# Kernel optimization log

Hardware: AMD Instinct MI355X
Metric: run time of the kernel (lower is better)

## Reference

```python
import jax, jax.numpy as jnp
import numpy as np
from jax import lax

B, C, T = 16, 32, 512
GAF_SIZE = 128
LATENT = 128
EPS = 1e-8


def _conv(x, w, b, stride):
    # x: (N, Cin, H, W), w: (Cout, Cin, kh, kw)
    y = lax.conv_general_dilated(x, w, (stride, stride), 'SAME',
                                 dimension_numbers=('NCHW', 'OIHW', 'NCHW'))
    return jax.nn.relu(y + b[None, :, None, None])


def _compute_gaf(x_raw):
    # x_raw: (B, C, T) -> (B*C, 2, S, S) with channels [GASF, GADF]
    S = GAF_SIZE
    # Piecewise Aggregate Approximation: T -> S
    x = x_raw.reshape(B, C, S, T // S).mean(axis=-1)        # (B, C, S)
    # Min-max normalize each series to [-1, 1]
    mn = x.min(axis=-1, keepdims=True)
    mx = x.max(axis=-1, keepdims=True)
    x = jnp.clip(2.0 * (x - mn) / (mx - mn + EPS) - 1.0, -1.0, 1.0)
    # phi = arccos(x); use trig identities to avoid explicit arccos
    sq = jnp.sqrt(jnp.clip(1.0 - x * x, 0.0, 1.0))          # sin(phi)
    xi, xj = x[..., :, None], x[..., None, :]
    si, sj = sq[..., :, None], sq[..., None, :]
    gasf = xi * xj - si * sj                                 # cos(phi_i + phi_j)
    gadf = si * xj - xi * sj                                 # sin(phi_i - phi_j)
    gaf = jnp.stack([gasf, gadf], axis=2)                    # (B, C, 2, S, S)
    return gaf.reshape(B * C, 2, S, S).astype(jnp.float32)


def _encoder(gaf, W1, b1, W2, b2, W3, b3, W4, b4, Wfc, bfc):
    h = _conv(gaf, W1, b1, 2)   # (B*C, 32, 64, 64)
    h = _conv(h, W2, b2, 2)     # (B*C, 64, 32, 32)
    h = _conv(h, W3, b3, 2)     # (B*C, 128, 16, 16)
    h = _conv(h, W4, b4, 2)     # (B*C, 256, 8, 8)
    h = h.mean(axis=(2, 3))     # global average pool -> (B*C, 256)
    return h @ Wfc + bfc        # (B*C, LATENT)


def setup_inputs() -> dict:
    key = jax.random.key(0)
    ks = jax.random.split(key, 12)
    p = lambda k, shp: (jax.random.normal(k, shp, dtype=jnp.float32) * 0.05)
    return {
        'x_raw': jax.random.normal(ks[0], (B, C, T), dtype=jnp.float32),
        'W1': p(ks[1], (32, 2, 3, 3)),   'b1': jnp.zeros((32,), jnp.float32),
        'W2': p(ks[2], (64, 32, 3, 3)),  'b2': jnp.zeros((64,), jnp.float32),
        'W3': p(ks[3], (128, 64, 3, 3)), 'b3': jnp.zeros((128,), jnp.float32),
        'W4': p(ks[4], (256, 128, 3, 3)),'b4': jnp.zeros((256,), jnp.float32),
        'Wfc': p(ks[5], (256, LATENT)),  'bfc': jnp.zeros((LATENT,), jnp.float32),
    }


def reference(x_raw, W1, b1, W2, b2, W3, b3, W4, b4, Wfc, bfc):
    # GAF computed from detached raw EEG in the original (numpy CPU path)
    gaf = lax.stop_gradient(_compute_gaf(x_raw))
    z = _encoder(gaf, W1, b1, W2, b2, W3, b3, W4, b4, Wfc, bfc)
    return z.reshape(B, C, LATENT).mean(axis=1)              # (B, LATENT)
```

## Files before the change

### kernel.cpp

```cpp
#include <hip/hip_runtime.h>
#include <hip/hip_bf16.h>

#define DEV __device__ __forceinline__

constexpr int kB = 16, kC = 32, kT = 512, kS = 128, kBC = 512, kLatent = 128;
constexpr float kEps = 1e-8f;

using bf16 = __hip_bfloat16;
using bf16x8 = __attribute__((ext_vector_type(8))) short;
using f32x4  = __attribute__((ext_vector_type(4))) float;

DEV unsigned short f2bf(float v) {
    bf16 h = __float2bfloat16(v);
    return *(unsigned short*)&h;
}

DEV void gld16(const void* g, void* l) {
    __builtin_amdgcn_global_load_lds(
        (const __attribute__((address_space(1))) unsigned*)g,
        (__attribute__((address_space(3))) unsigned*)l, 16, 0, 0);
}

__global__ void gaf_stats_kernel(const float* __restrict__ x_raw,
                                 float* __restrict__ xn, float* __restrict__ sq) {
    int bc = blockIdx.x;
    int s  = threadIdx.x;
    const float* xp = x_raw + (size_t)bc * kT;
    float v = 0.25f * (xp[4*s] + xp[4*s+1] + xp[4*s+2] + xp[4*s+3]);
    __shared__ float smn[kS], smx[kS];
    smn[s] = v; smx[s] = v;
    __syncthreads();
    for (int off = kS/2; off > 0; off >>= 1) {
        if (s < off) {
            smn[s] = fminf(smn[s], smn[s+off]);
            smx[s] = fmaxf(smx[s], smx[s+off]);
        }
        __syncthreads();
    }
    float mn = smn[0], mx = smx[0];
    float xv = 2.0f * (v - mn) / (mx - mn + kEps) - 1.0f;
    xv = fminf(fmaxf(xv, -1.0f), 1.0f);
    float sv = sqrtf(fminf(fmaxf(1.0f - xv*xv, 0.0f), 1.0f));
    xn[bc*kS + s] = xv;
    sq[bc*kS + s] = sv;
}

__global__ void wtrans_all_kernel(const float* __restrict__ w1,
                                  const float* __restrict__ w2,
                                  const float* __restrict__ w3,
                                  const float* __restrict__ w4,
                                  bf16* __restrict__ w1b, bf16* __restrict__ wt2,
                                  bf16* __restrict__ wt3, bf16* __restrict__ wt4) {
    int idx = blockIdx.x * blockDim.x + threadIdx.x;
    if (idx < 1024) {
        int oc = idx >> 5, k = idx & 31;
        w1b[idx] = __float2bfloat16(k < 18 ? w1[oc*18 + k] : 0.0f);
        return;
    }
    idx -= 1024;
    const float* src; bf16* dst; int CIN, COUT;
    if (idx < 18432)       { src = w2; dst = wt2; CIN = 32;  COUT = 64;  }
    else if (idx < 92160)  { idx -= 18432;  src = w3; dst = wt3; CIN = 64;  COUT = 128; }
    else if (idx < 387072) { idx -= 92160;  src = w4; dst = wt4; CIN = 128; COUT = 256; }
    else return;
    int ic = idx % CIN;
    int oc = (idx / CIN) % COUT;
    int t  = idx / (CIN * COUT);
    dst[((size_t)t * COUT + oc) * CIN + ic] = __float2bfloat16(src[((size_t)oc * CIN + ic) * 9 + t]);
}

__global__ __launch_bounds__(256, 4)
void conv12_kernel(const float* __restrict__ xn, const float* __restrict__ sq,
                   const bf16* __restrict__ w1b, const float* __restrict__ b1,
                   const bf16* __restrict__ wt2, const float* __restrict__ b2,
                   bf16* __restrict__ out, int img0) {
    __shared__ float xl[kS], sl[kS];
    __shared__ __align__(16) short GH[18432];
    __shared__ __align__(16) short W1s[32][40];

    int tid  = threadIdx.x;
    int lane = tid & 63;
    int wv   = tid >> 6;
    int mblk = blockIdx.x;
    int bz   = blockIdx.y;
    int bc   = img0 + bz;

    if (tid < 128) {
        xl[tid] = xn[(size_t)bc * kS + tid];
        int rr = tid >> 2, sg = tid & 3;
        *(uint4*)&W1s[rr][sg*8] = *(const uint4*)(w1b + rr*32 + sg*8);
    } else {
        sl[tid - 128] = sq[(size_t)bc * kS + (tid - 128)];
    }
    __syncthreads();

    #pragma unroll
    for (int it = 0; it < 3; ++it) {
        int idx = it * 256 + tid;
        if (idx >= 576) break;
        int trow = idx >> 6, hx = idx & 63;
        int iy = 8 * mblk + trow;
        unsigned int pk[16];
        #pragma unroll
        for (int j = 0; j < 16; ++j) pk[j] = 0u;
        if (iy < 64) {
            float xr[3], sr[3], xc[3], sc[3];
            #pragma unroll
            for (int k = 0; k < 3; ++k) {
                int iyy = 2*iy + k, ixx = 2*hx + k;
                bool vy = iyy < kS, vx = ixx < kS;
                xr[k] = vy ? xl[iyy] : 0.0f;  sr[k] = vy ? sl[iyy] : 0.0f;
                xc[k] = vx ? xl[ixx] : 0.0f;  sc[k] = vx ? sl[ixx] : 0.0f;
            }
            unsigned short gs[18];
            #pragma unroll
            for (int ky = 0; ky < 3; ++ky)
                #pragma unroll
                for (int kx = 0; kx < 3; ++kx) {
                    gs[ky*3+kx]   = f2bf(xr[ky]*xc[kx] - sr[ky]*sc[kx]);
                    gs[9+ky*3+kx] = f2bf(sr[ky]*xc[kx] - xr[ky]*sc[kx]);
                }
            #pragma unroll
            for (int j = 0; j < 9; ++j)
                pk[j] = (unsigned int)gs[2*j] | ((unsigned int)gs[2*j+1] << 16);
        }
        #pragma unroll
        for (int j = 0; j < 4; ++j)
            *(uint4*)&GH[idx*32 + ((j ^ (idx & 3)) * 8)] = ((uint4*)pk)[j];
    }
    __syncthreads();

    f32x4 c1[9][2];
    bf16x8 w1f0 = *(const bf16x8*)&W1s[(lane & 15)][(lane>>4)*8];
    bf16x8 w1f1 = *(const bf16x8*)&W1s[16 + (lane & 15)][(lane>>4)*8];
    #pragma unroll
    for (int j = 0; j < 9; ++j) {
        int mt = 4*j + wv;
        int row = mt*16 + (lane & 15);
        bf16x8 af = *(const bf16x8*)&GH[row*32 + (((lane>>4) ^ (row & 3)) * 8)];
        f32x4 zz = f32x4{0.f, 0.f, 0.f, 0.f};
        c1[j][0] = __builtin_amdgcn_mfma_f32_16x16x32_bf16(af, w1f0, zz, 0, 0, 0);
        c1[j][1] = __builtin_amdgcn_mfma_f32_16x16x32_bf16(af, w1f1, zz, 0, 0, 0);
    }
    __syncthreads();

    #pragma unroll
    for (int j = 0; j < 9; ++j) {
        int mt = 4*j + wv;
        #pragma unroll
        for (int h = 0; h < 2; ++h) {
            int oc = h*16 + (lane & 15);
            float bb = b1[oc];
            #pragma unroll
            for (int rg = 0; rg < 4; ++rg) {
                int pos = mt*16 + (lane>>4)*4 + rg;
                int trow = pos >> 6, hx = pos & 63;
                int par = hx & 1, col = hx >> 1;
                int r = trow*32 + col;
                float v = fmaxf(c1[j][h][rg] + bb, 0.0f);
                if (8*mblk + trow >= 64) v = 0.0f;
                GH[par*9216 + r*32 + (((oc>>3) ^ (r & 3)) * 8) + (oc & 7)] = (short)f2bf(v);
            }
        }
    }
    __syncthreads();

    auto loadB2 = [&](int tap, bf16x8* dst) {
        #pragma unroll
        for (int ni = 0; ni < 4; ++ni) {
            int row = ni*16 + (lane & 15);
            dst[ni] = *(const bf16x8*)(wt2 + ((size_t)tap*64 + row)*32 + (lane>>4)*8);
        }
    };
    f32x4 acc[2][4];
    #pragma unroll
    for (int i = 0; i < 2; ++i)
        #pragma unroll
        for (int j = 0; j < 4; ++j) acc[i][j] = f32x4{0.f, 0.f, 0.f, 0.f};

    bf16x8 bcur[4], bnxt[4];
    loadB2(0, bcur);
    for (int tap = 0; tap < 9; ++tap) {
        if (tap + 1 < 9) loadB2(tap + 1, bnxt);
        int ky = tap / 3, kx = tap % 3;
        int trow = 2*wv + ky;
        bf16x8 af[2];
        #pragma unroll
        for (int mi = 0; mi < 2; ++mi) {
            int ocol = mi*16 + (lane & 15);
            int x = 2*ocol + kx;
            int par = x & 1;
            int col = x >> 1; if (col > 31) col = 31;
            int r = trow*32 + col;
            bf16x8 v = *(const bf16x8*)&GH[par*9216 + r*32 + (((lane>>4) ^ (r & 3)) * 8)];
            bf16x8 z = {0,0,0,0,0,0,0,0};
            af[mi] = (x < 64) ? v : z;
        }
        #pragma unroll
        for (int mi = 0; mi < 2; ++mi)
            #pragma unroll
            for (int ni = 0; ni < 4; ++ni)
                acc[mi][ni] = __builtin_amdgcn_mfma_f32_16x16x32_bf16(af[mi], bcur[ni], acc[mi][ni], 0, 0, 0);
        #pragma unroll
        for (int ni = 0; ni < 4; ++ni) bcur[ni] = bnxt[ni];
    }

    int oy = 4*mblk + wv;
    #pragma unroll
    for (int ni = 0; ni < 4; ++ni) {
        int oc = ni*16 + (lane & 15);
        float b = b2[oc];
        #pragma unroll
        for (int mi = 0; mi < 2; ++mi)
            #pragma unroll
            for (int rg = 0; rg < 4; ++rg) {
                int ocol = 16*mi + (lane>>4)*4 + rg;
                float v = fmaxf(acc[mi][ni][rg] + b, 0.0f);
                out[(((size_t)bz*32 + oy)*32 + ocol)*64 + oc] = __float2bfloat16(v);
            }
    }
}

template<int CIN, int COUT, int HIN, int IMGS, bool POOL>
__global__ __launch_bounds__(256, 4)
void conv_mfma_kernel(const bf16* __restrict__ in, const bf16* __restrict__ wt,
                      const float* __restrict__ bias, bf16* __restrict__ out,
                      float* __restrict__ pooled, int img0,
                      const bf16* __restrict__ zbuf) {
    constexpr int HOUT = HIN / 2;
    constexpr int PPI  = HOUT * HOUT;
    constexpr int S    = 9 * (CIN / 32);
    __shared__ __align__(16) short As[2*128*32];
    __shared__ __align__(16) short Bs[2*128*32];

    int tid  = threadIdx.x;
    int lane = tid & 63;
    int wv   = tid >> 6;
    int wm   = wv >> 1, wn = wv & 1;
    int bx   = blockIdx.x;
    int nblk = blockIdx.y;
    int bz   = blockIdx.z;

    int rsub = lane >> 2, seg = lane & 3;
    int imgA[2], oyA[2], oxA[2], rB[2];
    #pragma unroll
    for (int j = 0; j < 2; ++j) {
        int r = (wv*2 + j)*16 + rsub;
        int il, pos;
        if (IMGS > 1) { il = bz*IMGS + r/PPI; pos = r % PPI; }
        else          { il = bz; pos = bx*128 + r; }
        imgA[j] = il; oyA[j] = pos / HOUT; oxA[j] = pos % HOUT;
        rB[j] = r;
    }

    auto issue = [&](int s, int nb) {
        int icb = (s / 9) * 32;
        int tap = s % 9;
        int ky = tap / 3, kx = tap % 3;
        #pragma unroll
        for (int j = 0; j < 2; ++j) {
            int iy = 2*oyA[j] + ky, ix = 2*oxA[j] + kx;
            const bf16* ga = (iy < HIN && ix < HIN)
                ? in + (((size_t)imgA[j]*HIN + iy)*HIN + ix)*CIN + icb + seg*8
                : zbuf + seg*8;
            gld16(ga, (char*)As + nb*8192 + (wv*2 + j)*1024 + lane*16);
            const bf16* gb = wt + ((size_t)tap*COUT + nblk*128 + rB[j])*CIN + icb + seg*8;
            gld16(gb, (char*)Bs + nb*8192 + (wv*2 + j)*1024 + lane*16);
        }
    };

    f32x4 acc[4][4];
    #pragma unroll
    for (int i = 0; i < 4; ++i)
        #pragma unroll
        for (int j = 0; j < 4; ++j) acc[i][j] = f32x4{0.f, 0.f, 0.f, 0.f};

    issue(0, 0);
    __syncthreads();

    for (int s = 0; s < S; ++s) {
        int cur = s & 1;
        if (s + 1 < S) issue(s + 1, cur ^ 1);
        bf16x8 af[4], bfr[4];
        #pragma unroll
        for (int mi = 0; mi < 4; ++mi)
            af[mi] = *(const bf16x8*)&As[cur*4096 + (wm*64 + mi*16 + (lane&15))*32 + (lane>>4)*8];
        #pragma unroll
        for (int ni = 0; ni < 4; ++ni)
            bfr[ni] = *(const bf16x8*)&Bs[cur*4096 + (wn*64 + ni*16 + (lane&15))*32 + (lane>>4)*8];
        #pragma unroll
        for (int mi = 0; mi < 4; ++mi)
            #pragma unroll
            for (int ni = 0; ni < 4; ++ni)
                acc[mi][ni] = __builtin_amdgcn_mfma_f32_16x16x32_bf16(af[mi], bfr[ni], acc[mi][ni], 0, 0, 0);
        __syncthreads();
    }

    if (!POOL) {
        #pragma unroll
        for (int ni = 0; ni < 4; ++ni) {
            int oc = nblk*128 + wn*64 + ni*16 + (lane & 15);
            float b = bias[oc];
            #pragma unroll
            for (int mi = 0; mi < 4; ++mi)
                #pragma unroll
                for (int rg = 0; rg < 4; ++rg) {
                    int rr = wm*64 + mi*16 + (lane>>4)*4 + rg;
                    int img_e, pos_e;
                    if (IMGS > 1) { img_e = bz*IMGS + rr/PPI; pos_e = rr % PPI; }
                    else          { img_e = bz; pos_e = bx*128 + rr; }
                    int oye = pos_e / HOUT, oxe = pos_e % HOUT;
                    float v = fmaxf(acc[mi][ni][rg] + b, 0.0f);
                    out[(((size_t)img_e * HOUT + oye) * HOUT + oxe) * COUT + oc] = __float2bfloat16(v);
                }
        }
    } else {
        int img_e = bz*IMGS + wm;
        #pragma unroll
        for (int ni = 0; ni < 4; ++ni) {
            int oc = nblk*128 + wn*64 + ni*16 + (lane & 15);
            float b = bias[oc];
            float s = 0.0f;
            #pragma unroll
            for (int mi = 0; mi < 4; ++mi)
                #pragma unroll
                for (int rg = 0; rg < 4; ++rg) s += fmaxf(acc[mi][ni][rg] + b, 0.0f);
            s += __shfl_xor(s, 16);
            s += __shfl_xor(s, 32);
            if (lane < 16)
                pooled[((size_t)(img0 + img_e))*256 + nblk*128 + wn*64 + ni*16 + lane] = s * (1.0f/64.0f);
        }
    }
}

__global__ void poolfc_kernel(const float* __restrict__ pooled, const float* __restrict__ Wfc,
                              const float* __restrict__ bfc, float* __restrict__ out) {
    int b = blockIdx.x;
    int t = threadIdx.x;
    __shared__ float pm[256];
    #pragma unroll
    for (int q = 0; q < 2; ++q) {
        int k = q*128 + t;
        float s = 0.0f;
        #pragma unroll
        for (int c = 0; c < kC; ++c) s += pooled[((size_t)(b*kC + c))*256 + k];
        pm[k] = s * (1.0f/kC);
    }
    __syncthreads();
    float acc = bfc[t];
    for (int k = 0; k < 256; ++k) acc = fmaf(pm[k], Wfc[(size_t)k*kLatent + t], acc);
    out[(size_t)b*kLatent + t] = acc;
}

extern "C" void kernel_launch(void* const* d_in, const int* in_sizes, int n_in,
                              void* d_out, int out_size, void* d_ws, size_t ws_size,
                              hipStream_t stream) {
    const float* x_raw = (const float*)d_in[0];
    const float* W1 = (const float*)d_in[1];  const float* b1 = (const float*)d_in[2];
    const float* W2 = (const float*)d_in[3];  const float* b2 = (const float*)d_in[4];
    const float* W3 = (const float*)d_in[5];  const float* b3 = (const float*)d_in[6];
    const float* W4 = (const float*)d_in[7];  const float* b4 = (const float*)d_in[8];
    const float* Wfc = (const float*)d_in[9]; const float* bfc = (const float*)d_in[10];
    float* out = (float*)d_out;

    char* wsb = (char*)d_ws;
    float* xn     = (float*)(wsb);
    float* sq     = (float*)(wsb + (256u<<10));
    float* pooled = (float*)(wsb + (512u<<10));
    bf16* Wt2     = (bf16*)(wsb + (1280u<<10));
    bf16* Wt3     = (bf16*)(wsb + (1316u<<10));
    bf16* Wt4     = (bf16*)(wsb + (1460u<<10));
    bf16* W1b     = (bf16*)(wsb + (2036u<<10));
    bf16* zbuf    = (bf16*)(wsb + (2040u<<10));
    char* chunk_base = wsb + (2048u<<10);

    const size_t perH2 = 32u*32u*64u*2u, perH3 = 16u*16u*128u*2u;
    const size_t perImg = perH2 + perH3;
    int chunk = 4;
    for (int c = 512; c >= 4; c >>= 1) {
        if ((2048u<<10) + (size_t)c * perImg <= ws_size) { chunk = c; break; }
    }

    hipMemsetAsync(zbuf, 0, 1024, stream);
    gaf_stats_kernel<<<kBC, kS, 0, stream>>>(x_raw, xn, sq);
    wtrans_all_kernel<<<(388096 + 255)/256, 256, 0, stream>>>(W1, W2, W3, W4, W1b, Wt2, Wt3, Wt4);

    for (int img0 = 0; img0 < kBC; img0 += chunk) {
        int nimg = chunk;
        bf16* h2 = (bf16*)chunk_base;
        bf16* h3 = (bf16*)(chunk_base + (size_t)chunk * perH2);

        conv12_kernel<<<dim3(8, nimg), 256, 0, stream>>>(xn, sq, W1b, b1, Wt2, b2, h2, img0);
        conv_mfma_kernel<64, 128, 32, 1, false>
            <<<dim3(2, 1, nimg), 256, 0, stream>>>(h2, Wt3, b3, h3, nullptr, img0, zbuf);
        conv_mfma_kernel<128, 256, 16, 2, true>
            <<<dim3(1, 2, nimg/2), 256, 0, stream>>>(h3, Wt4, b4, nullptr, pooled, img0, zbuf);
    }

    poolfc_kernel<<<kB, kLatent, 0, stream>>>(pooled, Wfc, bfc, out);
}
```

Before: 214.4 us.

## Merge prep kernels, pack bf16 conversion pairwise, deepen K-step in conv4

```diff
diff --git a/kernel.cpp b/kernel.cpp
--- a/kernel.cpp
+++ b/kernel.cpp
@@ -21,37 +21,41 @@
         (__attribute__((address_space(3))) unsigned*)l, 16, 0, 0);
 }
 
-__global__ void gaf_stats_kernel(const float* __restrict__ x_raw,
-                                 float* __restrict__ xn, float* __restrict__ sq) {
-    int bc = blockIdx.x;
-    int s  = threadIdx.x;
-    const float* xp = x_raw + (size_t)bc * kT;
-    float v = 0.25f * (xp[4*s] + xp[4*s+1] + xp[4*s+2] + xp[4*s+3]);
-    __shared__ float smn[kS], smx[kS];
-    smn[s] = v; smx[s] = v;
-    __syncthreads();
-    for (int off = kS/2; off > 0; off >>= 1) {
-        if (s < off) {
-            smn[s] = fminf(smn[s], smn[s+off]);
-            smx[s] = fmaxf(smx[s], smx[s+off]);
+__global__ void prep_kernel(const float* __restrict__ x_raw,
+                            const float* __restrict__ w1, const float* __restrict__ w2,
+                            const float* __restrict__ w3, const float* __restrict__ w4,
+                            float* __restrict__ xn, float* __restrict__ sq,
+                            bf16* __restrict__ w1b, bf16* __restrict__ wt2,
+                            bf16* __restrict__ wt3, bf16* __restrict__ wt4) {
+    int tid = threadIdx.x;
+    if (blockIdx.x < 512) {
+        __shared__ float smn[kS], smx[kS];
+        int bc = blockIdx.x;
+        float v = 0.0f;
+        if (tid < 128) {
+            const float* xp = x_raw + (size_t)bc * kT;
+            v = 0.25f * (xp[4*tid] + xp[4*tid+1] + xp[4*tid+2] + xp[4*tid+3]);
+            smn[tid] = v; smx[tid] = v;
         }
         __syncthreads();
-    }
-    float mn = smn[0], mx = smx[0];
-    float xv = 2.0f * (v - mn) / (mx - mn + kEps) - 1.0f;
-    xv = fminf(fmaxf(xv, -1.0f), 1.0f);
-    float sv = sqrtf(fminf(fmaxf(1.0f - xv*xv, 0.0f), 1.0f));
-    xn[bc*kS + s] = xv;
-    sq[bc*kS + s] = sv;
-}
-
-__global__ void wtrans_all_kernel(const float* __restrict__ w1,
-                                  const float* __restrict__ w2,
-                                  const float* __restrict__ w3,
-                                  const float* __restrict__ w4,
-                                  bf16* __restrict__ w1b, bf16* __restrict__ wt2,
-                                  bf16* __restrict__ wt3, bf16* __restrict__ wt4) {
-    int idx = blockIdx.x * blockDim.x + threadIdx.x;
+        for (int off = kS/2; off > 0; off >>= 1) {
+            if (tid < off) {
+                smn[tid] = fminf(smn[tid], smn[tid+off]);
+                smx[tid] = fmaxf(smx[tid], smx[tid+off]);
+            }
+            __syncthreads();
+        }
+        if (tid < 128) {
+            float mn = smn[0], mx = smx[0];
+            float xv = 2.0f * (v - mn) / (mx - mn + kEps) - 1.0f;
+            xv = fminf(fmaxf(xv, -1.0f), 1.0f);
+            float sv = sqrtf(fminf(fmaxf(1.0f - xv*xv, 0.0f), 1.0f));
+            xn[bc*kS + tid] = xv;
+            sq[bc*kS + tid] = sv;
+        }
+        return;
+    }
+    int idx = (blockIdx.x - 512) * blockDim.x + tid;
     if (idx < 1024) {
         int oc = idx >> 5, k = idx & 31;
         w1b[idx] = __float2bfloat16(k < 18 ? w1[oc*18 + k] : 0.0f);
@@ -112,17 +116,19 @@
                 xr[k] = vy ? xl[iyy] : 0.0f;  sr[k] = vy ? sl[iyy] : 0.0f;
                 xc[k] = vx ? xl[ixx] : 0.0f;  sc[k] = vx ? sl[ixx] : 0.0f;
             }
-            unsigned short gs[18];
+            float fg[18];
             #pragma unroll
             for (int ky = 0; ky < 3; ++ky)
                 #pragma unroll
                 for (int kx = 0; kx < 3; ++kx) {
-                    gs[ky*3+kx]   = f2bf(xr[ky]*xc[kx] - sr[ky]*sc[kx]);
-                    gs[9+ky*3+kx] = f2bf(sr[ky]*xc[kx] - xr[ky]*sc[kx]);
+                    fg[ky*3+kx]   = xr[ky]*xc[kx] - sr[ky]*sc[kx];
+                    fg[9+ky*3+kx] = sr[ky]*xc[kx] - xr[ky]*sc[kx];
                 }
             #pragma unroll
-            for (int j = 0; j < 9; ++j)
-                pk[j] = (unsigned int)gs[2*j] | ((unsigned int)gs[2*j+1] << 16);
+            for (int j = 0; j < 9; ++j) {
+                __hip_bfloat162 hh = __float22bfloat162_rn(make_float2(fg[2*j], fg[2*j+1]));
+                pk[j] = *(unsigned int*)&hh;
+            }
         }
         #pragma unroll
         for (int j = 0; j < 4; ++j)
@@ -221,7 +227,7 @@
     }
 }
 
-template<int CIN, int COUT, int HIN, int IMGS, bool POOL>
+template<int CIN, int COUT, int HIN, int IMGS, int KU, bool POOL>
 __global__ __launch_bounds__(256, 4)
 void conv_mfma_kernel(const bf16* __restrict__ in, const bf16* __restrict__ wt,
                       const float* __restrict__ bias, bf16* __restrict__ out,
@@ -229,9 +235,10 @@
                       const bf16* __restrict__ zbuf) {
     constexpr int HOUT = HIN / 2;
     constexpr int PPI  = HOUT * HOUT;
-    constexpr int S    = 9 * (CIN / 32);
-    __shared__ __align__(16) short As[2*128*32];
-    __shared__ __align__(16) short Bs[2*128*32];
+    constexpr int S32  = 9 * (CIN / 32);
+    constexpr int SO   = S32 / KU;
+    __shared__ __align__(16) short As[2*128*32*KU];
+    __shared__ __align__(16) short Bs[2*128*32*KU];
 
     int tid  = threadIdx.x;
     int lane = tid & 63;
@@ -253,19 +260,23 @@
         rB[j] = r;
     }
 
-    auto issue = [&](int s, int nb) {
-        int icb = (s / 9) * 32;
-        int tap = s % 9;
-        int ky = tap / 3, kx = tap % 3;
-        #pragma unroll
-        for (int j = 0; j < 2; ++j) {
-            int iy = 2*oyA[j] + ky, ix = 2*oxA[j] + kx;
-            const bf16* ga = (iy < HIN && ix < HIN)
-                ? in + (((size_t)imgA[j]*HIN + iy)*HIN + ix)*CIN + icb + seg*8
-                : zbuf + seg*8;
-            gld16(ga, (char*)As + nb*8192 + (wv*2 + j)*1024 + lane*16);
-            const bf16* gb = wt + ((size_t)tap*COUT + nblk*128 + rB[j])*CIN + icb + seg*8;
-            gld16(gb, (char*)Bs + nb*8192 + (wv*2 + j)*1024 + lane*16);
+    auto issue = [&](int so, int nb) {
+        #pragma unroll
+        for (int u = 0; u < KU; ++u) {
+            int s = so*KU + u;
+            int icb = (s / 9) * 32;
+            int tap = s % 9;
+            int ky = tap / 3, kx = tap % 3;
+            #pragma unroll
+            for (int j = 0; j < 2; ++j) {
+                int iy = 2*oyA[j] + ky, ix = 2*oxA[j] + kx;
+                const bf16* ga = (iy < HIN && ix < HIN)
+                    ? in + (((size_t)imgA[j]*HIN + iy)*HIN + ix)*CIN + icb + seg*8
+                    : zbuf + seg*8;
+                gld16(ga, (char*)As + (nb*KU + u)*8192 + (wv*2 + j)*1024 + lane*16);
+                const bf16* gb = wt + ((size_t)tap*COUT + nblk*128 + rB[j])*CIN + icb + seg*8;
+                gld16(gb, (char*)Bs + (nb*KU + u)*8192 + (wv*2 + j)*1024 + lane*16);
+            }
         }
     };
 
@@ -278,21 +289,24 @@
     issue(0, 0);
     __syncthreads();
 
-    for (int s = 0; s < S; ++s) {
-        int cur = s & 1;
-        if (s + 1 < S) issue(s + 1, cur ^ 1);
-        bf16x8 af[4], bfr[4];
-        #pragma unroll
-        for (int mi = 0; mi < 4; ++mi)
-            af[mi] = *(const bf16x8*)&As[cur*4096 + (wm*64 + mi*16 + (lane&15))*32 + (lane>>4)*8];
-        #pragma unroll
-        for (int ni = 0; ni < 4; ++ni)
-            bfr[ni] = *(const bf16x8*)&Bs[cur*4096 + (wn*64 + ni*16 + (lane&15))*32 + (lane>>4)*8];
-        #pragma unroll
-        for (int mi = 0; mi < 4; ++mi)
+    for (int so = 0; so < SO; ++so) {
+        int cur = so & 1;
+        if (so + 1 < SO) issue(so + 1, cur ^ 1);
+        #pragma unroll
+        for (int u = 0; u < KU; ++u) {
+            bf16x8 af[4], bfr[4];
+            #pragma unroll
+            for (int mi = 0; mi < 4; ++mi)
+                af[mi] = *(const bf16x8*)&As[(cur*KU + u)*4096 + (wm*64 + mi*16 + (lane&15))*32 + (lane>>4)*8];
             #pragma unroll
             for (int ni = 0; ni < 4; ++ni)
-                acc[mi][ni] = __builtin_amdgcn_mfma_f32_16x16x32_bf16(af[mi], bfr[ni], acc[mi][ni], 0, 0, 0);
+                bfr[ni] = *(const bf16x8*)&Bs[(cur*KU + u)*4096 + (wn*64 + ni*16 + (lane&15))*32 + (lane>>4)*8];
+            #pragma unroll
+            for (int mi = 0; mi < 4; ++mi)
+                #pragma unroll
+                for (int ni = 0; ni < 4; ++ni)
+                    acc[mi][ni] = __builtin_amdgcn_mfma_f32_16x16x32_bf16(af[mi], bfr[ni], acc[mi][ni], 0, 0, 0);
+        }
         __syncthreads();
     }
 
@@ -382,8 +396,8 @@
     }
 
     hipMemsetAsync(zbuf, 0, 1024, stream);
-    gaf_stats_kernel<<<kBC, kS, 0, stream>>>(x_raw, xn, sq);
-    wtrans_all_kernel<<<(388096 + 255)/256, 256, 0, stream>>>(W1, W2, W3, W4, W1b, Wt2, Wt3, Wt4);
+    prep_kernel<<<512 + (388096 + 255)/256, 256, 0, stream>>>(
+        x_raw, W1, W2, W3, W4, xn, sq, W1b, Wt2, Wt3, Wt4);
 
     for (int img0 = 0; img0 < kBC; img0 += chunk) {
         int nimg = chunk;
@@ -391,9 +405,9 @@
         bf16* h3 = (bf16*)(chunk_base + (size_t)chunk * perH2);
 
         conv12_kernel<<<dim3(8, nimg), 256, 0, stream>>>(xn, sq, W1b, b1, Wt2, b2, h2, img0);
-        conv_mfma_kernel<64, 128, 32, 1, false>
+        conv_mfma_kernel<64, 128, 32, 1, 1, false>
             <<<dim3(2, 1, nimg), 256, 0, stream>>>(h2, Wt3, b3, h3, nullptr, img0, zbuf);
-        conv_mfma_kernel<128, 256, 16, 2, true>
+        conv_mfma_kernel<128, 256, 16, 2, 2, true>
             <<<dim3(1, 2, nimg/2), 256, 0, stream>>>(h3, Wt4, b4, nullptr, pooled, img0, zbuf);
     }
 
```

New measurement: 207.3 us. -3.3%, faster.
